# Performance work log

Hardware: AMD Instinct MI355X
Metric: run time of the kernel (lower is better)

Reference implementation:

```python
import jax, jax.numpy as jnp
import numpy as np

IN_FEATURES = 100000
OUT_FEATURES = 100000
NNZ = 1600000
BATCH = 64


def setup_inputs() -> dict:
    key = jax.random.key(0)
    k1, k2, k3, k4, k5 = jax.random.split(key, 5)
    x = jax.random.normal(k1, (BATCH, IN_FEATURES), dtype=jnp.float32)
    values = jax.random.normal(k2, (NNZ,), dtype=jnp.float32)
    bias = jax.random.normal(k3, (OUT_FEATURES,), dtype=jnp.float32)
    # torch COO is coalesced -> row indices sorted (rows = dst of transposed matrix)
    rows = jnp.sort(jax.random.randint(k4, (NNZ,), 0, OUT_FEATURES, dtype=jnp.int64))
    cols = jax.random.randint(k5, (NNZ,), 0, IN_FEATURES, dtype=jnp.int64)
    return {"x": x, "values": values, "bias": bias, "rows": rows, "cols": cols}


def reference(x, values, bias, rows, cols):
    # out = x @ conn  <=>  out.T = conn_T @ x.T, conn_T given in COO (rows=dst, cols=src)
    # gather source activations along edges: (nnz, B)
    contrib = x[:, cols].T * values[:, None]
    # scatter-add into destinations: (out_features, B)
    out_t = jax.ops.segment_sum(contrib, rows, num_segments=OUT_FEATURES,
                                indices_are_sorted=True)
    return out_t.T + bias  # (B, out_features)
```

## Files before the change

kernel.cpp:

```cpp
#include <hip/hip_runtime.h>
#include <hip/hip_fp16.h>

#define IN_F   100000
#define OUT_F  100000
#define NNZ_N  1600000
#define TC     256
#define TBLK   ((IN_F + TC - 1) / TC)
#define SBLK   ((NNZ_N + 255) / 256)
#define RBLK   ((OUT_F + 63) / 64)
#define ED_CAP 2048

__device__ __forceinline__ float2 h2f(unsigned u) {
    const __half2 h = *reinterpret_cast<const __half2*>(&u);
    return __half22float2(h);
}

#define EDGE_FMA(U, V) do { float2 f_;                                         \
    f_ = h2f((U).x); acc[0] = fmaf((V), f_.x, acc[0]); acc[1] = fmaf((V), f_.y, acc[1]); \
    f_ = h2f((U).y); acc[2] = fmaf((V), f_.x, acc[2]); acc[3] = fmaf((V), f_.y, acc[3]); \
    f_ = h2f((U).z); acc[4] = fmaf((V), f_.x, acc[4]); acc[5] = fmaf((V), f_.y, acc[5]); \
    f_ = h2f((U).w); acc[6] = fmaf((V), f_.x, acc[6]); acc[7] = fmaf((V), f_.y, acc[7]); \
} while (0)

__global__ __launch_bounds__(256) void k_prep(
    const float* __restrict__ x,
    const int*   __restrict__ rows,
    unsigned* __restrict__ xh,
    int*      __restrict__ rstart) {
    __shared__ unsigned tile[TC][33];
    const int bid = blockIdx.x;
    const int t   = threadIdx.x;

    if (bid < TBLK) {
        const int i0   = bid * TC;
        const int colr = i0 + t;
        if (colr < IN_F) {
            #pragma unroll 8
            for (int p = 0; p < 32; ++p) {
                const float a = x[(size_t)(2 * p)     * IN_F + colr];
                const float b = x[(size_t)(2 * p + 1) * IN_F + colr];
                const __half2 h = __floats2half2_rn(a, b);
                tile[t][p] = *reinterpret_cast<const unsigned*>(&h);
            }
        }
        __syncthreads();
        const int u  = t & 31;
        const int c8 = t >> 5;
        for (int cc = c8; cc < TC; cc += 8) {
            const int col = i0 + cc;
            if (col < IN_F)
                xh[(size_t)col * 32 + u] = tile[cc][u];
        }
    } else {
        const int e = (bid - TBLK) * 256 + t;
        if (e >= NNZ_N) return;
        const int cur  = rows[e];
        const int prev = (e == 0) ? -1 : rows[e - 1];
        for (int r = prev + 1; r <= cur; ++r) rstart[r] = e;
        if (e == NNZ_N - 1)
            for (int r = cur + 1; r <= OUT_F; ++r) rstart[r] = NNZ_N;
    }
}

__global__ __launch_bounds__(512, 4) void k_spmm(
    const uint4* __restrict__ xh4,
    const int*   __restrict__ rstart,
    const int*   __restrict__ cols,
    const float* __restrict__ vals,
    const float* __restrict__ bias,
    float* __restrict__ out) {
    __shared__ int   rs[65];
    __shared__ int   ecol[ED_CAP];
    __shared__ float eval[ED_CAP];
    __shared__ float tile[64][65];
    const int r0   = blockIdx.x * 64;
    const int t    = threadIdx.x;
    const int lane = t & 63;
    const int w    = t >> 6;

    if (t < 65) {
        int idx = r0 + t; if (idx > OUT_F) idx = OUT_F;
        rs[t] = rstart[idx];
    }
    __syncthreads();

    const int s  = rs[0];
    const int ne = rs[64] - s;
    const int ns = (ne < ED_CAP) ? ne : ED_CAP;
    for (int i = t; i < ns; i += 512) {
        ecol[i] = cols[s + i];
        eval[i] = vals[s + i];
    }
    __syncthreads();

    const int gg  = t >> 3;
    const int sub = t & 7;
    const int ls  = rs[gg]     - s;
    const int n   = rs[gg + 1] - s;

    float acc[8];
    #pragma unroll
    for (int i = 0; i < 8; ++i) acc[i] = 0.f;

    if (ne <= ED_CAP) {
        for (int base = ls; base < n; base += 8) {
            int c[8]; float v[8];
            #pragma unroll
            for (int j = 0; j < 8; ++j) {
                const int i = (base + j < n) ? base + j : n - 1;
                c[j] = ecol[i];
                v[j] = (base + j < n) ? eval[i] : 0.f;
            }
            uint4 u[8];
            #pragma unroll
            for (int j = 0; j < 8; ++j)
                u[j] = xh4[(size_t)c[j] * 8 + sub];
            #pragma unroll
            for (int j = 0; j < 8; ++j)
                EDGE_FMA(u[j], v[j]);
        }
    } else {
        for (int base = ls; base < n; base += 8) {
            int c[8]; float v[8];
            #pragma unroll
            for (int j = 0; j < 8; ++j) {
                const int i = (base + j < n) ? base + j : n - 1;
                c[j] = cols[s + i];
                v[j] = (base + j < n) ? vals[s + i] : 0.f;
            }
            uint4 u[8];
            #pragma unroll
            for (int j = 0; j < 8; ++j)
                u[j] = xh4[(size_t)c[j] * 8 + sub];
            #pragma unroll
            for (int j = 0; j < 8; ++j)
                EDGE_FMA(u[j], v[j]);
        }
    }

    #pragma unroll
    for (int i = 0; i < 8; ++i) tile[gg][(sub << 3) + i] = acc[i];
    __syncthreads();

    const int rc = r0 + lane;
    if (rc < OUT_F) {
        const float bv = bias[rc];
        for (int bb = w; bb < 64; bb += 8)
            out[(size_t)bb * OUT_F + rc] = tile[lane][bb] + bv;
    }
}

__global__ __launch_bounds__(256) void k_spmm_fallback(
    const float* __restrict__ x,
    const float* __restrict__ vals,
    const int*   __restrict__ rows,
    const int*   __restrict__ cols,
    const float* __restrict__ bias,
    float* __restrict__ out) {
    __shared__ int   rstart[65];
    __shared__ float tile[64][65];
    const int r0   = blockIdx.x * 64;
    const int t    = threadIdx.x;
    const int lane = t & 63;
    const int w    = t >> 6;
    if (t < 65) {
        const int target = r0 + t;
        int lo = 0, hi = NNZ_N;
        while (lo < hi) {
            const int mid = (lo + hi) >> 1;
            if (rows[mid] < target) lo = mid + 1; else hi = mid;
        }
        rstart[t] = lo;
    }
    __syncthreads();
    for (int j = w; j < 64; j += 4) {
        const int s = rstart[j], e = rstart[j + 1];
        float acc = 0.f;
        const size_t base = (size_t)lane * IN_F;
        for (int idx = s; idx < e; ++idx)
            acc = fmaf(vals[idx], x[base + cols[idx]], acc);
        tile[j][lane] = acc;
    }
    __syncthreads();
    const int c = lane;
    if (r0 + c < OUT_F) {
        const float bv = bias[r0 + c];
        for (int bb = w; bb < 64; bb += 4)
            out[(size_t)bb * OUT_F + (r0 + c)] = tile[c][bb] + bv;
    }
}

extern "C" void kernel_launch(void* const* d_in, const int* in_sizes, int n_in,
                              void* d_out, int out_size, void* d_ws, size_t ws_size,
                              hipStream_t stream) {
    const float* x      = (const float*)d_in[0];
    const float* values = (const float*)d_in[1];
    const float* bias   = (const float*)d_in[2];
    const int*   rows   = (const int*)d_in[3];
    const int*   cols   = (const int*)d_in[4];
    float*       out    = (float*)d_out;

    const size_t xh_bytes = (size_t)IN_F * 32 * sizeof(unsigned);
    const size_t rs_off   = (xh_bytes + 255) & ~(size_t)255;
    const size_t need     = rs_off + (size_t)(OUT_F + 1) * sizeof(int);

    if (ws_size >= need) {
        unsigned* xh     = (unsigned*)d_ws;
        int*      rstart = (int*)((char*)d_ws + rs_off);
        k_prep<<<TBLK + SBLK, 256, 0, stream>>>(x, rows, xh, rstart);
        k_spmm<<<RBLK, 512, 0, stream>>>((const uint4*)xh, rstart, cols, values, bias, out);
    } else {
        k_spmm_fallback<<<RBLK, 256, 0, stream>>>(x, values, rows, cols, bias, out);
    }
}
```

Baseline: 127.9 us.

## Split fp16 activation table into four batch slabs and gather per slab pass

The transposed fp16 activation table is reorganized into four slabs of 16 batch columns each, and the SpMM kernel loops over the slabs in separate passes. Each thread now gathers 4 bytes per edge instead of a 16-byte vector. The aim is to shrink the gather working set per pass so it stays resident in L2. The cost is re-reading the edge lists four times and issuing four times as many narrower, less coalesced gather loads. Since blocks are not synchronized across passes, the effective working set may stay mixed anyway.

```diff
diff --git a/kernel.cpp b/kernel.cpp
--- a/kernel.cpp
+++ b/kernel.cpp
@@ -1,26 +1,21 @@
 #include <hip/hip_runtime.h>
 #include <hip/hip_fp16.h>
 
-#define IN_F   100000
-#define OUT_F  100000
-#define NNZ_N  1600000
-#define TC     256
-#define TBLK   ((IN_F + TC - 1) / TC)
-#define SBLK   ((NNZ_N + 255) / 256)
-#define RBLK   ((OUT_F + 63) / 64)
-#define ED_CAP 2048
+#define IN_F     100000
+#define OUT_F    100000
+#define NNZ_N    1600000
+#define TC       256
+#define TBLK     ((IN_F + TC - 1) / TC)
+#define SBLK     ((NNZ_N + 255) / 256)
+#define RBLK     ((OUT_F + 63) / 64)
+#define ED_CAP   2048
+#define NPASS    4
+#define SLAB_U32 ((size_t)IN_F * 8)
 
 __device__ __forceinline__ float2 h2f(unsigned u) {
     const __half2 h = *reinterpret_cast<const __half2*>(&u);
     return __half22float2(h);
 }
-
-#define EDGE_FMA(U, V) do { float2 f_;                                         \
-    f_ = h2f((U).x); acc[0] = fmaf((V), f_.x, acc[0]); acc[1] = fmaf((V), f_.y, acc[1]); \
-    f_ = h2f((U).y); acc[2] = fmaf((V), f_.x, acc[2]); acc[3] = fmaf((V), f_.y, acc[3]); \
-    f_ = h2f((U).z); acc[4] = fmaf((V), f_.x, acc[4]); acc[5] = fmaf((V), f_.y, acc[5]); \
-    f_ = h2f((U).w); acc[6] = fmaf((V), f_.x, acc[6]); acc[7] = fmaf((V), f_.y, acc[7]); \
-} while (0)
 
 __global__ __launch_bounds__(256) void k_prep(
     const float* __restrict__ x,
@@ -46,10 +41,12 @@
         __syncthreads();
         const int u  = t & 31;
         const int c8 = t >> 5;
+        unsigned* slab = xh + (size_t)(u >> 3) * SLAB_U32;
+        const int q  = u & 7;
         for (int cc = c8; cc < TC; cc += 8) {
             const int col = i0 + cc;
             if (col < IN_F)
-                xh[(size_t)col * 32 + u] = tile[cc][u];
+                slab[(size_t)col * 8 + q] = tile[cc][u];
         }
     } else {
         const int e = (bid - TBLK) * 256 + t;
@@ -63,7 +60,7 @@
 }
 
 __global__ __launch_bounds__(512, 4) void k_spmm(
-    const uint4* __restrict__ xh4,
+    const unsigned* __restrict__ xh,
     const int*   __restrict__ rstart,
     const int*   __restrict__ cols,
     const float* __restrict__ vals,
@@ -103,43 +100,66 @@
     for (int i = 0; i < 8; ++i) acc[i] = 0.f;
 
     if (ne <= ED_CAP) {
-        for (int base = ls; base < n; base += 8) {
-            int c[8]; float v[8];
-            #pragma unroll
-            for (int j = 0; j < 8; ++j) {
-                const int i = (base + j < n) ? base + j : n - 1;
-                c[j] = ecol[i];
-                v[j] = (base + j < n) ? eval[i] : 0.f;
+        #pragma unroll
+        for (int p = 0; p < NPASS; ++p) {
+            const unsigned* __restrict__ slab = xh + (size_t)p * SLAB_U32;
+            float a0 = 0.f, a1 = 0.f;
+            for (int base = ls; base < n; base += 8) {
+                int c[8]; float v[8];
+                #pragma unroll
+                for (int j = 0; j < 8; ++j) {
+                    const int i = (base + j < n) ? base + j : n - 1;
+                    c[j] = ecol[i];
+                    v[j] = (base + j < n) ? eval[i] : 0.f;
+                }
+                unsigned u[8];
+                #pragma unroll
+                for (int j = 0; j < 8; ++j)
+                    u[j] = slab[(size_t)c[j] * 8 + sub];
+                #pragma unroll
+                for (int j = 0; j < 8; ++j) {
+                    const float2 f = h2f(u[j]);
+                    a0 = fmaf(v[j], f.x, a0);
+                    a1 = fmaf(v[j], f.y, a1);
+                }
             }
-            uint4 u[8];
-            #pragma unroll
-            for (int j = 0; j < 8; ++j)
-                u[j] = xh4[(size_t)c[j] * 8 + sub];
-            #pragma unroll
-            for (int j = 0; j < 8; ++j)
-                EDGE_FMA(u[j], v[j]);
+            acc[2 * p]     = a0;
+            acc[2 * p + 1] = a1;
         }
     } else {
-        for (int base = ls; base < n; base += 8) {
-            int c[8]; float v[8];
-            #pragma unroll
-            for (int j = 0; j < 8; ++j) {
-                const int i = (base + j < n) ? base + j : n - 1;
-                c[j] = cols[s + i];
-                v[j] = (base + j < n) ? vals[s + i] : 0.f;
+        #pragma unroll
+        for (int p = 0; p < NPASS; ++p) {
+            const unsigned* __restrict__ slab = xh + (size_t)p * SLAB_U32;
+            float a0 = 0.f, a1 = 0.f;
+            for (int base = ls; base < n; base += 8) {
+                int c[8]; float v[8];
+                #pragma unroll
+                for (int j = 0; j < 8; ++j) {
+                    const int i = (base + j < n) ? base + j : n - 1;
+                    c[j] = cols[s + i];
+                    v[j] = (base + j < n) ? vals[s + i] : 0.f;
+                }
+                unsigned u[8];
+                #pragma unroll
+                for (int j = 0; j < 8; ++j)
+                    u[j] = slab[(size_t)c[j] * 8 + sub];
+                #pragma unroll
+                for (int j = 0; j < 8; ++j) {
+                    const float2 f = h2f(u[j]);
+                    a0 = fmaf(v[j], f.x, a0);
+                    a1 = fmaf(v[j], f.y, a1);
+                }
             }
-            uint4 u[8];
-            #pragma unroll
-            for (int j = 0; j < 8; ++j)
-                u[j] = xh4[(size_t)c[j] * 8 + sub];
-            #pragma unroll
-            for (int j = 0; j < 8; ++j)
-                EDGE_FMA(u[j], v[j]);
+            acc[2 * p]     = a0;
+            acc[2 * p + 1] = a1;
         }
     }
 
     #pragma unroll
-    for (int i = 0; i < 8; ++i) tile[gg][(sub << 3) + i] = acc[i];
+    for (int p = 0; p < NPASS; ++p) {
+        tile[gg][16 * p + 2 * sub]     = acc[2 * p];
+        tile[gg][16 * p + 2 * sub + 1] = acc[2 * p + 1];
+    }
     __syncthreads();
 
     const int rc = r0 + lane;
@@ -200,7 +220,7 @@
     const int*   cols   = (const int*)d_in[4];
     float*       out    = (float*)d_out;
 
-    const size_t xh_bytes = (size_t)IN_F * 32 * sizeof(unsigned);
+    const size_t xh_bytes = (size_t)NPASS * SLAB_U32 * sizeof(unsigned);
     const size_t rs_off   = (xh_bytes + 255) & ~(size_t)255;
     const size_t need     = rs_off + (size_t)(OUT_F + 1) * sizeof(int);
 
@@ -208,7 +228,7 @@
         unsigned* xh     = (unsigned*)d_ws;
         int*      rstart = (int*)((char*)d_ws + rs_off);
         k_prep<<<TBLK + SBLK, 256, 0, stream>>>(x, rows, xh, rstart);
-        k_spmm<<<RBLK, 512, 0, stream>>>((const uint4*)xh, rstart, cols, values, bias, out);
+        k_spmm<<<RBLK, 512, 0, stream>>>(xh, rstart, cols, values, bias, out);
     } else {
         k_spmm_fallback<<<RBLK, 256, 0, stream>>>(x, values, rows, cols, bias, out);
     }
```

Measured after the change: 169.5 us. 32.6% more time.
